# Performance work log

Measured on AMD Instinct MI355X. Metric: run time of the kernel, lower is better.

## Reference

```python
import jax, jax.numpy as jnp
import numpy as np

T_LEN = 1024
N_IN = 512
BATCH = 32
SURR_ALPHA = 4.0  # slope of the sigmoid surrogate gradient


@jax.custom_vjp
def heaviside_sg(x):
    # spike = Heaviside(x); backward uses sigmoid surrogate derivative
    return (x >= 0).astype(x.dtype)

def _hs_fwd(x):
    return heaviside_sg(x), x

def _hs_bwd(x, g):
    s = jax.nn.sigmoid(SURR_ALPHA * x)
    return (g * SURR_ALPHA * s * (1.0 - s),)

heaviside_sg.defvjp(_hs_fwd, _hs_bwd)


def setup_inputs() -> dict:
    key = jax.random.key(0)
    k1, k2, k3 = jax.random.split(key, 3)
    current = jax.random.normal(k1, (T_LEN, BATCH, N_IN), dtype=jnp.float32)
    beta = jax.random.uniform(k2, (N_IN,), dtype=jnp.float32)  # per-channel decay in (0,1)
    v_init = jax.random.normal(k3, (BATCH, N_IN), dtype=jnp.float32)
    v_th = jnp.ones((T_LEN, BATCH, N_IN), dtype=jnp.float32)
    return {"current": current, "beta": beta, "v_init": v_init, "v_th": v_th}


def reference(current, beta, v_init, v_th):
    # Torch version: grouped causal conv1d with kernel beta^{T-1-k}, i.e.
    # membrane[t] = sum_{j<=t} beta^{t-j} * current[j], with current[0] += beta*v_init.
    # Equivalent O(T) linear recurrence: m_t = beta*m_{t-1} + c_t, m_{-1}=v_init.
    def step(m, c):
        m = beta * m + c  # beta (N,) broadcasts over (B,N)
        return m, m

    m_last, membrane = jax.lax.scan(step, v_init, current)  # membrane: (T,B,N)

    # surrogate-gradient spike function
    spikes = heaviside_sg(membrane - v_th)  # (T,B,N)

    # triangular phi kernel: z[t] = sum_{j<=t} (t-j+1)*spikes[j] == double cumsum
    z = jnp.cumsum(jnp.cumsum(spikes, axis=0), axis=0)  # (T,B,N)

    # Block.g: keep entries equal to 1, zero everything else; gradient is identity
    # (the subtracted term is detached in the torch code).
    gz = z - jax.lax.stop_gradient(jnp.where(z == 1.0, 0.0, z))

    return gz, z, m_last  # m_last == membrane[:, :, -1] in torch layout (B,N)
```

## Files before the change

kernel.cpp:

```cpp
#include <hip/hip_runtime.h>


#define T_LEN 1024
#define N_IN  512
#define BN    16384
#define SEG_T 32
#define NSEG  (T_LEN / SEG_T)

__global__ __launch_bounds__(576, 1) void snn_fused(
        const float* __restrict__ cur, const float* __restrict__ beta,
        const float* __restrict__ vini, const float* __restrict__ vth,
        float* __restrict__ gz, float* __restrict__ zo, float* __restrict__ ml)
{
    __shared__ float zbuf[2][SEG_T][64];

    const int lane   = threadIdx.x & 63;
    const int wave   = threadIdx.x >> 6;
    const int chbase = blockIdx.x * 64;

    if (wave == 0) {
        const int i = chbase + lane;
        const float bta = beta[i & (N_IN - 1)];
        float m = vini[i];
        int C = 0, Z = 0;
        const float* __restrict__ cp = cur + i;
        const float* __restrict__ vp = vth + i;

        float cA[SEG_T], vA[SEG_T], cB[SEG_T], vB[SEG_T];

#pragma unroll
        for (int t = 0; t < SEG_T; ++t) {
            cA[t] = cp[(size_t)t * BN];
            vA[t] = vp[(size_t)t * BN];
        }

        auto step = [&](float (&Xc)[SEG_T], float (&Xv)[SEG_T],
                        float (&Yc)[SEG_T], float (&Yv)[SEG_T],
                        int segNext, float* zb) {
            asm volatile("s_waitcnt vmcnt(0)" ::: "memory");
            if (segNext < NSEG) {
                const float* __restrict__ c2 = cp + (size_t)segNext * SEG_T * BN;
                const float* __restrict__ v2 = vp + (size_t)segNext * SEG_T * BN;
#pragma unroll
                for (int t = 0; t < SEG_T; ++t) {
                    Yc[t] = c2[(size_t)t * BN];
                    Yv[t] = v2[(size_t)t * BN];
                }
            }
            __builtin_amdgcn_sched_barrier(0);
#pragma unroll
            for (int t = 0; t < SEG_T; ++t) {
                m = fmaf(bta, m, Xc[t]);
                const int sp = (m >= Xv[t]) ? 1 : 0;
                C += sp;
                Z += C;
                zb[t * 64] = (float)Z;
            }
            asm volatile("s_waitcnt lgkmcnt(0)" ::: "memory");
        };

        step(cA, vA, cB, vB, 1, &zbuf[0][0][lane]);
        __builtin_amdgcn_s_barrier();
#pragma unroll 1
        for (int k = 0; k < (NSEG - 2) / 2; ++k) {
            step(cB, vB, cA, vA, 2 * k + 2, &zbuf[1][0][lane]);
            __builtin_amdgcn_s_barrier();
            step(cA, vA, cB, vB, 2 * k + 3, &zbuf[0][0][lane]);
            __builtin_amdgcn_s_barrier();
        }
        step(cB, vB, cA, vA, NSEG, &zbuf[1][0][lane]);
        ml[i] = m;
        __builtin_amdgcn_s_barrier();
    } else {
        const int ww      = wave - 1;
        const int row_sub = lane >> 4;
        const int chgrp   = lane & 15;
        const int myrow   = 4 * ww + row_sub;

#pragma unroll 1
        for (int n = 0; n < NSEG; ++n) {
            __builtin_amdgcn_s_barrier();
            const float4 zq = *reinterpret_cast<const float4*>(
                                  &zbuf[n & 1][myrow][4 * chgrp]);
            const float4 gf = make_float4(zq.x == 1.0f ? 1.0f : 0.0f,
                                          zq.y == 1.0f ? 1.0f : 0.0f,
                                          zq.z == 1.0f ? 1.0f : 0.0f,
                                          zq.w == 1.0f ? 1.0f : 0.0f);
            const size_t off = (size_t)(n * 32 + myrow) * BN
                             + chbase + 4 * chgrp;
            *reinterpret_cast<float4*>(gz + off) = gf;
            *reinterpret_cast<float4*>(zo + off) = zq;
        }
    }
}

extern "C" void kernel_launch(void* const* d_in, const int* in_sizes, int n_in,
                              void* d_out, int out_size, void* d_ws, size_t ws_size,
                              hipStream_t stream) {
    const float* cur  = (const float*)d_in[0];
    const float* beta = (const float*)d_in[1];
    const float* vini = (const float*)d_in[2];
    const float* vth  = (const float*)d_in[3];
    float* gz = (float*)d_out;
    float* zo = gz + (size_t)T_LEN * BN;
    float* ml = zo + (size_t)T_LEN * BN;

    snn_fused<<<BN / 64, 576, 0, stream>>>(cur, beta, vini, vth, gz, zo, ml);
}
```

Before: 239.3 us.

## Replace barrier double-buffer with LDS ring and flag-based producer/consumer sync

The producer wave now works on 8-step segments with four register slots in flight. It publishes each finished segment into a 16-slot LDS ring through a volatile ready counter instead of a block-wide s_barrier. Four store waves (down from eight) poll that counter and handle segments round-robin, reporting progress through per-wave done counters that the producer checks before reusing a ring slot. This decouples the serial scan from the store waves and keeps more global loads in flight. The cost is spin-wait polling on LDS flags and reliance on volatile LDS ordering for correctness.

```diff
diff --git a/kernel.cpp b/kernel.cpp
--- a/kernel.cpp
+++ b/kernel.cpp
@@ -4,19 +4,27 @@
 #define T_LEN 1024
 #define N_IN  512
 #define BN    16384
-#define SEG_T 32
-#define NSEG  (T_LEN / SEG_T)
+#define ST    8
+#define NSEG  (T_LEN / ST)
+#define RING  16
+#define NW    4
 
-__global__ __launch_bounds__(576, 1) void snn_fused(
+__global__ __launch_bounds__(320, 1) void snn_fused(
         const float* __restrict__ cur, const float* __restrict__ beta,
         const float* __restrict__ vini, const float* __restrict__ vth,
         float* __restrict__ gz, float* __restrict__ zo, float* __restrict__ ml)
 {
-    __shared__ float zbuf[2][SEG_T][64];
+    __shared__ float zring[RING][ST][64];
+    __shared__ volatile int seg_ready;
+    __shared__ volatile int wdone[NW];
 
     const int lane   = threadIdx.x & 63;
     const int wave   = threadIdx.x >> 6;
     const int chbase = blockIdx.x * 64;
+
+    if (threadIdx.x == 0) seg_ready = 0;
+    if (threadIdx.x < NW) wdone[threadIdx.x] = 0;
+    __syncthreads();
 
     if (wave == 0) {
         const int i = chbase + lane;
@@ -26,70 +34,90 @@
         const float* __restrict__ cp = cur + i;
         const float* __restrict__ vp = vth + i;
 
-        float cA[SEG_T], vA[SEG_T], cB[SEG_T], vB[SEG_T];
+        float c0[ST], v0[ST], c1[ST], v1[ST];
+        float c2[ST], v2[ST], c3[ST], v3[ST];
 
-#pragma unroll
-        for (int t = 0; t < SEG_T; ++t) {
-            cA[t] = cp[(size_t)t * BN];
-            vA[t] = vp[(size_t)t * BN];
+#define LOADW(cw, vw, q) do {                                              \
+        const float* __restrict__ _c = cp + (size_t)(q) * ST * BN;         \
+        const float* __restrict__ _v = vp + (size_t)(q) * ST * BN;         \
+        _Pragma("unroll")                                                  \
+        for (int _t = 0; _t < ST; ++_t) {                                  \
+            cw[_t] = _c[(size_t)_t * BN];                                  \
+            vw[_t] = _v[(size_t)_t * BN];                                  \
+        } } while (0)
+
+#define CHAINW(cw, vw, s) do {                                             \
+        float* _zb = &zring[(s) & (RING - 1)][0][lane];                    \
+        _Pragma("unroll")                                                  \
+        for (int _t = 0; _t < ST; ++_t) {                                  \
+            m = fmaf(bta, m, cw[_t]);                  \
+            const int _sp = (m >= vw[_t]) ? 1 : 0;                         \
+            C += _sp;                                 \
+            Z += C;                                    \
+            _zb[_t * 64] = (float)Z;                                       \
+        }                                                                  \
+        asm volatile("s_waitcnt lgkmcnt(0)" ::: "memory");                 \
+        seg_ready = (s) + 1; } while (0)
+
+#define REFILL(cw, vw, s) do {                                             \
+        const int _q = (s) + 4;                                            \
+        if (_q < NSEG) {                                                   \
+            if (_q >= RING) {                                              \
+                const int _r = _q & (NW - 1);                              \
+                const int _need = (_q >> 2) - 3;   \
+                while (wdone[_r] < _need) __builtin_amdgcn_s_sleep(1);     \
+            }                                                              \
+            LOADW(cw, vw, _q);                                             \
+        } } while (0)
+
+        LOADW(c0, v0, 0); LOADW(c1, v1, 1);
+        LOADW(c2, v2, 2); LOADW(c3, v3, 3);
+
+#pragma unroll 1
+        for (int k = 0; k < NSEG / 4; ++k) {
+            const int s = 4 * k;
+            CHAINW(c0, v0, s);     REFILL(c0, v0, s);
+            CHAINW(c1, v1, s + 1); REFILL(c1, v1, s + 1);
+            CHAINW(c2, v2, s + 2); REFILL(c2, v2, s + 2);
+            CHAINW(c3, v3, s + 3); REFILL(c3, v3, s + 3);
         }
-
-        auto step = [&](float (&Xc)[SEG_T], float (&Xv)[SEG_T],
-                        float (&Yc)[SEG_T], float (&Yv)[SEG_T],
-                        int segNext, float* zb) {
-            asm volatile("s_waitcnt vmcnt(0)" ::: "memory");
-            if (segNext < NSEG) {
-                const float* __restrict__ c2 = cp + (size_t)segNext * SEG_T * BN;
-                const float* __restrict__ v2 = vp + (size_t)segNext * SEG_T * BN;
-#pragma unroll
-                for (int t = 0; t < SEG_T; ++t) {
-                    Yc[t] = c2[(size_t)t * BN];
-                    Yv[t] = v2[(size_t)t * BN];
-                }
-            }
-            __builtin_amdgcn_sched_barrier(0);
-#pragma unroll
-            for (int t = 0; t < SEG_T; ++t) {
-                m = fmaf(bta, m, Xc[t]);
-                const int sp = (m >= Xv[t]) ? 1 : 0;
-                C += sp;
-                Z += C;
-                zb[t * 64] = (float)Z;
-            }
-            asm volatile("s_waitcnt lgkmcnt(0)" ::: "memory");
-        };
-
-        step(cA, vA, cB, vB, 1, &zbuf[0][0][lane]);
-        __builtin_amdgcn_s_barrier();
-#pragma unroll 1
-        for (int k = 0; k < (NSEG - 2) / 2; ++k) {
-            step(cB, vB, cA, vA, 2 * k + 2, &zbuf[1][0][lane]);
-            __builtin_amdgcn_s_barrier();
-            step(cA, vA, cB, vB, 2 * k + 3, &zbuf[0][0][lane]);
-            __builtin_amdgcn_s_barrier();
-        }
-        step(cB, vB, cA, vA, NSEG, &zbuf[1][0][lane]);
         ml[i] = m;
-        __builtin_amdgcn_s_barrier();
+#undef LOADW
+#undef CHAINW
+#undef REFILL
     } else {
-        const int ww      = wave - 1;
+        const int w       = wave - 1;
         const int row_sub = lane >> 4;
         const int chgrp   = lane & 15;
-        const int myrow   = 4 * ww + row_sub;
+        int cnt = 0;
 
-#pragma unroll 1
-        for (int n = 0; n < NSEG; ++n) {
-            __builtin_amdgcn_s_barrier();
-            const float4 zq = *reinterpret_cast<const float4*>(
-                                  &zbuf[n & 1][myrow][4 * chgrp]);
-            const float4 gf = make_float4(zq.x == 1.0f ? 1.0f : 0.0f,
-                                          zq.y == 1.0f ? 1.0f : 0.0f,
-                                          zq.z == 1.0f ? 1.0f : 0.0f,
-                                          zq.w == 1.0f ? 1.0f : 0.0f);
-            const size_t off = (size_t)(n * 32 + myrow) * BN
-                             + chbase + 4 * chgrp;
-            *reinterpret_cast<float4*>(gz + off) = gf;
-            *reinterpret_cast<float4*>(zo + off) = zq;
+        for (int s = w; s < NSEG; s += NW) {
+            while (seg_ready <= s) __builtin_amdgcn_s_sleep(1);
+            asm volatile("" ::: "memory");
+            const int sl = s & (RING - 1);
+            const float4 za = *reinterpret_cast<const float4*>(
+                                  &zring[sl][row_sub][4 * chgrp]);
+            const float4 zb = *reinterpret_cast<const float4*>(
+                                  &zring[sl][row_sub + 4][4 * chgrp]);
+            asm volatile("s_waitcnt lgkmcnt(0)" ::: "memory");
+            ++cnt;
+            wdone[w] = cnt;
+
+            const float4 ga = make_float4(za.x == 1.0f ? 1.0f : 0.0f,
+                                          za.y == 1.0f ? 1.0f : 0.0f,
+                                          za.z == 1.0f ? 1.0f : 0.0f,
+                                          za.w == 1.0f ? 1.0f : 0.0f);
+            const float4 gb = make_float4(zb.x == 1.0f ? 1.0f : 0.0f,
+                                          zb.y == 1.0f ? 1.0f : 0.0f,
+                                          zb.z == 1.0f ? 1.0f : 0.0f,
+                                          zb.w == 1.0f ? 1.0f : 0.0f);
+            const size_t offa = (size_t)(s * ST + row_sub) * BN
+                              + chbase + 4 * chgrp;
+            const size_t offb = offa + (size_t)4 * BN;
+            *reinterpret_cast<float4*>(gz + offa) = ga;
+            *reinterpret_cast<float4*>(gz + offb) = gb;
+            *reinterpret_cast<float4*>(zo + offa) = za;
+            *reinterpret_cast<float4*>(zo + offb) = zb;
         }
     }
 }
@@ -105,5 +133,5 @@
     float* zo = gz + (size_t)T_LEN * BN;
     float* ml = zo + (size_t)T_LEN * BN;
 
-    snn_fused<<<BN / 64, 576, 0, stream>>>(cur, beta, vini, vth, gz, zo, ml);
+    snn_fused<<<BN / 64, 320, 0, stream>>>(cur, beta, vini, vth, gz, zo, ml);
 }
```

Result: slower. 294.8 us (+23.2%).
